# Kernel tuning notes

Hardware: AMD Instinct MI355X
Metric: run time of the kernel (lower is better)

## Reference

```python
import jax, jax.numpy as jnp
import numpy as np

N_NODES = 100000
N_EDGES = 1000000
D_IN = 64
D_OUT = 64


def setup_inputs() -> dict:
    key = jax.random.key(0)
    k_feat, k_ei, k_ew, k_w, k_b = jax.random.split(key, 5)
    features = jax.random.normal(k_feat, (N_NODES, D_IN), dtype=jnp.float32)
    edge_index = jax.random.randint(k_ei, (2, N_EDGES), 0, N_NODES, dtype=jnp.int64)
    edge_weight = jax.random.uniform(k_ew, (N_EDGES,), dtype=jnp.float32)
    # nn.Linear(input_dim, output_dim): weight [out, in], bias [out]
    lim = 1.0 / np.sqrt(D_IN)
    W = jax.random.uniform(k_w, (D_OUT, D_IN), minval=-lim, maxval=lim, dtype=jnp.float32)
    b = jax.random.uniform(k_b, (D_OUT,), minval=-lim, maxval=lim, dtype=jnp.float32)
    return {"features": features, "edge_index": edge_index,
            "edge_weight": edge_weight, "W": W, "b": b}


def reference(features, edge_index, edge_weight, W, b):
    # gather source-node features and scale by edge weight: [E, F]
    messages = features[edge_index[0]] * edge_weight[:, None]
    # scatter-add into destination nodes (vectorized form of the per-column
    # scatter_add_ loop in the original): [N, F]
    aggregated = jax.ops.segment_sum(messages, edge_index[1],
                                     num_segments=features.shape[0])
    # residual + linear; dropout is identity in eval mode
    return (aggregated + features) @ W.T + b
```

## Files before the change

### kernel.cpp

```cpp
#include <hip/hip_runtime.h>

constexpr int N_NODES = 100000;
constexpr int N_EDGES = 1000000;
constexpr int D = 64;
constexpr int NTILES = (N_NODES + 1023) / 1024;
constexpr int CAP = 32;
constexpr int OVF_CAP = 65536;


__global__ __launch_bounds__(256) void build_k(
    const int*   __restrict__ ei,
    const float* __restrict__ ew,
    int*         __restrict__ cnt,
    unsigned*    __restrict__ buckets,
    int*         __restrict__ ovfCount,
    int4*        __restrict__ ovf)
{
    int e = blockIdx.x * 256 + threadIdx.x;
    if (e >= N_EDGES) return;
    int   src = ei[e];
    int   dst = ei[N_EDGES + e];
    float w   = ew[e];
    int pos = atomicAdd(&cnt[dst], 1);
    if (pos < CAP) {
        unsigned q = (unsigned)(w * 32767.0f + 0.5f);
        buckets[(size_t)dst * CAP + pos] = ((unsigned)src << 15) | q;
    } else {
        int oi = atomicAdd(ovfCount, 1);
        if (oi < OVF_CAP) ovf[oi] = make_int4(dst, src, __float_as_int(w), 0);
    }
}

__global__ __launch_bounds__(256) void agg_gemm_bucket_k(
    const float*    __restrict__ feat,
    const unsigned* __restrict__ buckets,
    const int*      __restrict__ cnt,
    const int*      __restrict__ ovfCount,
    const int4*     __restrict__ ovf,
    const float*    __restrict__ W,
    const float*    __restrict__ bias,
    float*          __restrict__ out)
{
    constexpr int PITCH = 68;
    constexpr int NPB = 16;
    __shared__ float Wl[D * PITCH];
    __shared__ float xs[NPB][D];

    int tid = threadIdx.x;
    for (int i = tid; i < D * D; i += 256)
        Wl[(i >> 6) * PITCH + (i & 63)] = W[i];

    int lane = tid & 63;
    int wv   = tid >> 6;
    int g    = lane >> 4;
    int sub  = lane & 15;

    int slot = wv * 4 + g;
    int n    = blockIdx.x * NPB + slot;

    float4 acc = *reinterpret_cast<const float4*>(feat + (size_t)n * D + sub * 4);

    int degRaw = cnt[n];
    int deg = degRaw > CAP ? CAP : degRaw;
    const unsigned* ep = buckets + (size_t)n * CAP;
#pragma unroll 2
    for (int j = 0; j < deg; ++j) {
        unsigned r = ep[j];
        float w  = (float)(r & 0x7FFFu) * (1.0f / 32767.0f);
        int   s  = (int)(r >> 15);
        float4 f = *reinterpret_cast<const float4*>(
            feat + (size_t)s * D + sub * 4);
        acc.x = fmaf(f.x, w, acc.x);
        acc.y = fmaf(f.y, w, acc.y);
        acc.z = fmaf(f.z, w, acc.z);
        acc.w = fmaf(f.w, w, acc.w);
    }
    if (degRaw > CAP) {
        int m = *ovfCount;
        if (m > OVF_CAP) m = OVF_CAP;
        for (int i = 0; i < m; ++i) {
            int4 r = ovf[i];
            if (r.x == n) {
                float w  = __int_as_float(r.z);
                float4 f = *reinterpret_cast<const float4*>(
                    feat + (size_t)r.y * D + sub * 4);
                acc.x = fmaf(f.x, w, acc.x);
                acc.y = fmaf(f.y, w, acc.y);
                acc.z = fmaf(f.z, w, acc.z);
                acc.w = fmaf(f.w, w, acc.w);
            }
        }
    }
    *reinterpret_cast<float4*>(&xs[slot][sub * 4]) = acc;
    __syncthreads();

    const float4* w4 = reinterpret_cast<const float4*>(&Wl[lane * PITCH]);
    const float4* x0 = reinterpret_cast<const float4*>(&xs[wv * 4 + 0][0]);
    const float4* x1 = reinterpret_cast<const float4*>(&xs[wv * 4 + 1][0]);
    const float4* x2 = reinterpret_cast<const float4*>(&xs[wv * 4 + 2][0]);
    const float4* x3 = reinterpret_cast<const float4*>(&xs[wv * 4 + 3][0]);
    float b = bias[lane];
    float a0 = b, a1 = b, a2 = b, a3 = b;
#pragma unroll
    for (int i = 0; i < 16; ++i) {
        float4 wq = w4[i];
        float4 v0 = x0[i];
        float4 v1 = x1[i];
        float4 v2 = x2[i];
        float4 v3 = x3[i];
        a0 += v0.x * wq.x + v0.y * wq.y + v0.z * wq.z + v0.w * wq.w;
        a1 += v1.x * wq.x + v1.y * wq.y + v1.z * wq.z + v1.w * wq.w;
        a2 += v2.x * wq.x + v2.y * wq.y + v2.z * wq.z + v2.w * wq.w;
        a3 += v3.x * wq.x + v3.y * wq.y + v3.z * wq.z + v3.w * wq.w;
    }
    int nb = blockIdx.x * NPB + wv * 4;
    out[(size_t)(nb + 0) * D + lane] = a0;
    out[(size_t)(nb + 1) * D + lane] = a1;
    out[(size_t)(nb + 2) * D + lane] = a2;
    out[(size_t)(nb + 3) * D + lane] = a3;
}


__global__ __launch_bounds__(256) void rank_k(
    const int* __restrict__ ei, int* __restrict__ cnt, int* __restrict__ rank)
{
    int e = blockIdx.x * 256 + threadIdx.x;
    if (e >= N_EDGES) return;
    rank[e] = atomicAdd(&cnt[ei[N_EDGES + e]], 1);
}

__global__ __launch_bounds__(256) void tile_sum_k(
    const int* __restrict__ counts, int* __restrict__ tileSums)
{
    __shared__ int red[256];
    int t = threadIdx.x;
    int base = blockIdx.x * 1024 + t * 4;
    int4 c = make_int4(0, 0, 0, 0);
    if (base + 3 < N_NODES) {
        c = *reinterpret_cast<const int4*>(counts + base);
    } else {
        if (base + 0 < N_NODES) c.x = counts[base + 0];
        if (base + 1 < N_NODES) c.y = counts[base + 1];
        if (base + 2 < N_NODES) c.z = counts[base + 2];
        if (base + 3 < N_NODES) c.w = counts[base + 3];
    }
    red[t] = c.x + c.y + c.z + c.w;
    __syncthreads();
    for (int d = 128; d > 0; d >>= 1) {
        if (t < d) red[t] += red[t + d];
        __syncthreads();
    }
    if (t == 0) tileSums[blockIdx.x] = red[0];
}

__global__ __launch_bounds__(128) void tile_scan_k(
    const int* __restrict__ tileSums, int* __restrict__ tileBase)
{
    __shared__ int s[128];
    int t = threadIdx.x;
    s[t] = (t < NTILES) ? tileSums[t] : 0;
    __syncthreads();
    for (int d = 1; d < 128; d <<= 1) {
        int v = (t >= d) ? s[t - d] : 0;
        __syncthreads();
        s[t] += v;
        __syncthreads();
    }
    if (t < NTILES) tileBase[t] = t ? s[t - 1] : 0;
}

__global__ __launch_bounds__(256) void scan_apply_k(
    int* __restrict__ counts, const int* __restrict__ tileBase,
    int* __restrict__ offsets)
{
    __shared__ int tsum[256];
    int t = threadIdx.x;
    int base = blockIdx.x * 1024 + t * 4;
    int4 c = make_int4(0, 0, 0, 0);
    bool full = (base + 3 < N_NODES);
    if (full) {
        c = *reinterpret_cast<const int4*>(counts + base);
    } else {
        if (base + 0 < N_NODES) c.x = counts[base + 0];
        if (base + 1 < N_NODES) c.y = counts[base + 1];
        if (base + 2 < N_NODES) c.z = counts[base + 2];
        if (base + 3 < N_NODES) c.w = counts[base + 3];
    }
    tsum[t] = c.x + c.y + c.z + c.w;
    __syncthreads();
    for (int d = 1; d < 256; d <<= 1) {
        int v = (t >= d) ? tsum[t - d] : 0;
        __syncthreads();
        tsum[t] += v;
        __syncthreads();
    }
    int run = tileBase[blockIdx.x] + (t ? tsum[t - 1] : 0);
    int4 o = make_int4(run, run + c.x, run + c.x + c.y, run + c.x + c.y + c.z);
    if (full) {
        *reinterpret_cast<int4*>(offsets + base) = o;
        *reinterpret_cast<int4*>(counts  + base) = o;
    } else {
        if (base + 0 < N_NODES) { offsets[base + 0] = o.x; counts[base + 0] = o.x; }
        if (base + 1 < N_NODES) { offsets[base + 1] = o.y; counts[base + 1] = o.y; }
        if (base + 2 < N_NODES) { offsets[base + 2] = o.z; counts[base + 2] = o.z; }
        if (base + 3 < N_NODES) { offsets[base + 3] = o.w; counts[base + 3] = o.w; }
    }
    if (blockIdx.x == 0 && t == 0) offsets[N_NODES] = N_EDGES;
}

__global__ __launch_bounds__(256) void place_k(
    const int*   __restrict__ ei,
    const float* __restrict__ ew,
    const int*   __restrict__ rank,
    const int*   __restrict__ offsets,
    int2*        __restrict__ sorted_e)
{
    int e = blockIdx.x * 256 + threadIdx.x;
    if (e >= N_EDGES) return;
    int dst = ei[N_EDGES + e];
    int pos = offsets[dst] + rank[e];
    sorted_e[pos] = make_int2(ei[e], __float_as_int(ew[e]));
}

__global__ __launch_bounds__(256) void agg_gemm_k(
    const float* __restrict__ feat,
    const int2*  __restrict__ sorted_e,
    const int*   __restrict__ offsets,
    const float* __restrict__ W,
    const float* __restrict__ bias,
    float*       __restrict__ out)
{
    constexpr int PITCH = 68;
    constexpr int NPB = 16;
    __shared__ float Wl[D * PITCH];
    __shared__ float xs[NPB][D];

    int tid = threadIdx.x;
    for (int i = tid; i < D * D; i += 256)
        Wl[(i >> 6) * PITCH + (i & 63)] = W[i];

    int lane = tid & 63;
    int wv   = tid >> 6;
    int g    = lane >> 4;
    int sub  = lane & 15;

    int slot = wv * 4 + g;
    int n    = blockIdx.x * NPB + slot;
    int lo = offsets[n], hi = offsets[n + 1];
    int deg = hi - lo;

    float4 acc = *reinterpret_cast<const float4*>(feat + (size_t)n * D + sub * 4);

    const int2* ep = sorted_e + lo;
#pragma unroll 2
    for (int j = 0; j < deg; ++j) {
        int2  er = ep[j];
        float w  = __int_as_float(er.y);
        float4 f = *reinterpret_cast<const float4*>(
            feat + (size_t)er.x * D + sub * 4);
        acc.x = fmaf(f.x, w, acc.x);
        acc.y = fmaf(f.y, w, acc.y);
        acc.z = fmaf(f.z, w, acc.z);
        acc.w = fmaf(f.w, w, acc.w);
    }
    *reinterpret_cast<float4*>(&xs[slot][sub * 4]) = acc;
    __syncthreads();

    const float4* w4 = reinterpret_cast<const float4*>(&Wl[lane * PITCH]);
    const float4* x0 = reinterpret_cast<const float4*>(&xs[wv * 4 + 0][0]);
    const float4* x1 = reinterpret_cast<const float4*>(&xs[wv * 4 + 1][0]);
    const float4* x2 = reinterpret_cast<const float4*>(&xs[wv * 4 + 2][0]);
    const float4* x3 = reinterpret_cast<const float4*>(&xs[wv * 4 + 3][0]);
    float b = bias[lane];
    float a0 = b, a1 = b, a2 = b, a3 = b;
#pragma unroll
    for (int i = 0; i < 16; ++i) {
        float4 wq = w4[i];
        float4 v0 = x0[i];
        float4 v1 = x1[i];
        float4 v2 = x2[i];
        float4 v3 = x3[i];
        a0 += v0.x * wq.x + v0.y * wq.y + v0.z * wq.z + v0.w * wq.w;
        a1 += v1.x * wq.x + v1.y * wq.y + v1.z * wq.z + v1.w * wq.w;
        a2 += v2.x * wq.x + v2.y * wq.y + v2.z * wq.z + v2.w * wq.w;
        a3 += v3.x * wq.x + v3.y * wq.y + v3.z * wq.z + v3.w * wq.w;
    }
    int nb = blockIdx.x * NPB + wv * 4;
    out[(size_t)(nb + 0) * D + lane] = a0;
    out[(size_t)(nb + 1) * D + lane] = a1;
    out[(size_t)(nb + 2) * D + lane] = a2;
    out[(size_t)(nb + 3) * D + lane] = a3;
}


__global__ __launch_bounds__(256) void scatter_k(
    const float* __restrict__ feat,
    const int*   __restrict__ ei,
    const float* __restrict__ ew,
    float*       __restrict__ agg)
{
    int gid = blockIdx.x * 256 + threadIdx.x;
    int e = gid >> 4;
    if (e >= N_EDGES) return;
    int c = (gid & 15) * 4;
    int   src = ei[e];
    int   dst = ei[N_EDGES + e];
    float w   = ew[e];
    float4 f = *reinterpret_cast<const float4*>(feat + (size_t)src * D + c);
    float* a = agg + (size_t)dst * D + c;
    atomicAdd(a + 0, f.x * w);
    atomicAdd(a + 1, f.y * w);
    atomicAdd(a + 2, f.z * w);
    atomicAdd(a + 3, f.w * w);
}

__global__ __launch_bounds__(256) void gemm_k(
    const float* __restrict__ agg,
    const float* __restrict__ feat,
    const float* __restrict__ W,
    const float* __restrict__ bias,
    float*       __restrict__ out)
{
    constexpr int PITCH = 68;
    __shared__ float Wl[D * PITCH];
    __shared__ float xs[4][D];
    int tid = threadIdx.x;
    for (int i = tid; i < D * D; i += 256)
        Wl[(i >> 6) * PITCH + (i & 63)] = W[i];
    int o  = tid & 63;
    int wv = tid >> 6;
    int n  = blockIdx.x * 4 + wv;
    float b = bias[o];
    if (n < N_NODES)
        xs[wv][o] = agg[(size_t)n * D + o] + feat[(size_t)n * D + o];
    __syncthreads();
    if (n >= N_NODES) return;
    const float4* x4 = reinterpret_cast<const float4*>(&xs[wv][0]);
    const float4* w4 = reinterpret_cast<const float4*>(&Wl[o * PITCH]);
    float acc = b;
#pragma unroll
    for (int i = 0; i < 16; ++i) {
        float4 xv = x4[i];
        float4 wq = w4[i];
        acc += xv.x * wq.x + xv.y * wq.y + xv.z * wq.z + xv.w * wq.w;
    }
    out[(size_t)n * D + o] = acc;
}


extern "C" void kernel_launch(void* const* d_in, const int* in_sizes, int n_in,
                              void* d_out, int out_size, void* d_ws, size_t ws_size,
                              hipStream_t stream) {
    const float* feat = (const float*)d_in[0];
    const int*   ei   = (const int*)d_in[1];
    const float* ew   = (const float*)d_in[2];
    const float* W    = (const float*)d_in[3];
    const float* b    = (const float*)d_in[4];
    float*       out  = (float*)d_out;

    constexpr size_t NPAD = 100352;

    constexpr size_t CNT_OFF    = 0;
    constexpr size_t BUCKET_OFF = NPAD * sizeof(int);
    constexpr size_t OVF_OFF    = BUCKET_OFF + (size_t)N_NODES * CAP * sizeof(unsigned);
    constexpr size_t WS_BUCKET  = OVF_OFF + (size_t)OVF_CAP * sizeof(int4);

    constexpr size_t OFFSET_OFF = NPAD * sizeof(int);
    constexpr size_t RANK_OFF   = 2 * NPAD * sizeof(int);
    constexpr size_t SORT_OFF   = RANK_OFF + (size_t)N_EDGES * sizeof(int);
    constexpr size_t WS_SORT    = SORT_OFF + (size_t)N_EDGES * sizeof(int2);

    if (ws_size >= WS_BUCKET) {
        int*      cnt      = (int*)((char*)d_ws + CNT_OFF);
        int*      ovfCount = cnt + 100104;
        unsigned* buckets  = (unsigned*)((char*)d_ws + BUCKET_OFF);
        int4*     ovf      = (int4*)((char*)d_ws + OVF_OFF);

        hipMemsetAsync(cnt, 0, (100104 + 1) * sizeof(int), stream);
        build_k<<<(N_EDGES + 255) / 256, 256, 0, stream>>>(
            ei, ew, cnt, buckets, ovfCount, ovf);
        agg_gemm_bucket_k<<<N_NODES / 16, 256, 0, stream>>>(
            feat, buckets, cnt, ovfCount, ovf, W, b, out);
    } else if (ws_size >= WS_SORT) {
        int*  cnt      = (int*)((char*)d_ws + CNT_OFF);
        int*  offsets  = (int*)((char*)d_ws + OFFSET_OFF);
        int*  rank     = (int*)((char*)d_ws + RANK_OFF);
        int2* sorted_e = (int2*)((char*)d_ws + SORT_OFF);
        int*  tileSums = cnt + 100096;
        int*  tileBase = cnt + 100224;

        hipMemsetAsync(cnt, 0, N_NODES * sizeof(int), stream);
        rank_k     <<<(N_EDGES + 255) / 256, 256, 0, stream>>>(ei, cnt, rank);
        tile_sum_k <<<NTILES, 256, 0, stream>>>(cnt, tileSums);
        tile_scan_k<<<1, 128, 0, stream>>>(tileSums, tileBase);
        scan_apply_k<<<NTILES, 256, 0, stream>>>(cnt, tileBase, offsets);
        place_k    <<<(N_EDGES + 255) / 256, 256, 0, stream>>>(ei, ew, rank, offsets, sorted_e);
        agg_gemm_k <<<N_NODES / 16, 256, 0, stream>>>(feat, sorted_e, offsets, W, b, out);
    } else {
        const size_t agg_bytes = (size_t)N_NODES * D * sizeof(float);
        float* agg = (ws_size >= agg_bytes) ? (float*)d_ws : out;
        hipMemsetAsync(agg, 0, agg_bytes, stream);
        scatter_k<<<(N_EDGES * 16) / 256, 256, 0, stream>>>(feat, ei, ew, agg);
        gemm_k<<<(N_NODES + 3) / 4, 256, 0, stream>>>(agg, feat, W, b, out);
    }
}
```

Measured before the change: 210.0 us.

## Partition bucket build by destination range per XCD and split buckets into two halves

The build kernel becomes a grid-stride loop of 512 blocks. Each group of blocks (blockIdx mod 8) handles only edges whose destination falls in its 12500-node range. The intent is to keep the count atomics and bucket writes for a node range within one XCD's L2, reducing cross-die atomic and coherence traffic. The 32-slot per-node bucket is also split into a primary 16-slot array and a secondary 16-slot array, so the common low-degree case touches a denser 64-byte bucket. In exchange, every group reads the full destination index array (8x reads of that array), and the scheme relies on round-robin block-to-XCD dispatch.

```diff
diff --git a/kernel.cpp b/kernel.cpp
--- a/kernel.cpp
+++ b/kernel.cpp
@@ -4,36 +4,50 @@
 constexpr int N_EDGES = 1000000;
 constexpr int D = 64;
 constexpr int NTILES = (N_NODES + 1023) / 1024;
-constexpr int CAP = 32;
+constexpr int CAP1 = 16;
+constexpr int CAP2 = 16;
 constexpr int OVF_CAP = 65536;
+constexpr int NXCD = 8;
+constexpr int NODES_PER_GRP = 12500;
 
 
 __global__ __launch_bounds__(256) void build_k(
     const int*   __restrict__ ei,
     const float* __restrict__ ew,
     int*         __restrict__ cnt,
-    unsigned*    __restrict__ buckets,
+    unsigned*    __restrict__ b16,
+    unsigned*    __restrict__ b32,
     int*         __restrict__ ovfCount,
     int4*        __restrict__ ovf)
 {
-    int e = blockIdx.x * 256 + threadIdx.x;
-    if (e >= N_EDGES) return;
-    int   src = ei[e];
-    int   dst = ei[N_EDGES + e];
-    float w   = ew[e];
-    int pos = atomicAdd(&cnt[dst], 1);
-    if (pos < CAP) {
-        unsigned q = (unsigned)(w * 32767.0f + 0.5f);
-        buckets[(size_t)dst * CAP + pos] = ((unsigned)src << 15) | q;
-    } else {
-        int oi = atomicAdd(ovfCount, 1);
-        if (oi < OVF_CAP) ovf[oi] = make_int4(dst, src, __float_as_int(w), 0);
+    int grp  = blockIdx.x & 7;
+    int gidx = blockIdx.x >> 3;
+    int lo   = grp * NODES_PER_GRP;
+    int hi   = lo + NODES_PER_GRP;
+    int stride = (gridDim.x >> 3) * 256;
+
+    for (int e = gidx * 256 + threadIdx.x; e < N_EDGES; e += stride) {
+        int dst = ei[N_EDGES + e];
+        if (dst < lo || dst >= hi) continue;
+        int   src = ei[e];
+        float w   = ew[e];
+        unsigned rec = ((unsigned)src << 15) | (unsigned)(w * 32767.0f + 0.5f);
+        int pos = atomicAdd(&cnt[dst], 1);
+        if (pos < CAP1) {
+            b16[dst * 16 + pos] = rec;
+        } else if (pos < CAP1 + CAP2) {
+            b32[dst * 16 + (pos - CAP1)] = rec;
+        } else {
+            int oi = atomicAdd(ovfCount, 1);
+            if (oi < OVF_CAP) ovf[oi] = make_int4(dst, src, __float_as_int(w), 0);
+        }
     }
 }
 
 __global__ __launch_bounds__(256) void agg_gemm_bucket_k(
     const float*    __restrict__ feat,
-    const unsigned* __restrict__ buckets,
+    const unsigned* __restrict__ b16,
+    const unsigned* __restrict__ b32,
     const int*      __restrict__ cnt,
     const int*      __restrict__ ovfCount,
     const int4*     __restrict__ ovf,
@@ -61,8 +75,8 @@
     float4 acc = *reinterpret_cast<const float4*>(feat + (size_t)n * D + sub * 4);
 
     int degRaw = cnt[n];
-    int deg = degRaw > CAP ? CAP : degRaw;
-    const unsigned* ep = buckets + (size_t)n * CAP;
+    int deg = degRaw > CAP1 ? CAP1 : degRaw;
+    const unsigned* ep = b16 + (size_t)n * 16;
 #pragma unroll 2
     for (int j = 0; j < deg; ++j) {
         unsigned r = ep[j];
@@ -75,19 +89,34 @@
         acc.z = fmaf(f.z, w, acc.z);
         acc.w = fmaf(f.w, w, acc.w);
     }
-    if (degRaw > CAP) {
-        int m = *ovfCount;
-        if (m > OVF_CAP) m = OVF_CAP;
-        for (int i = 0; i < m; ++i) {
-            int4 r = ovf[i];
-            if (r.x == n) {
-                float w  = __int_as_float(r.z);
-                float4 f = *reinterpret_cast<const float4*>(
-                    feat + (size_t)r.y * D + sub * 4);
-                acc.x = fmaf(f.x, w, acc.x);
-                acc.y = fmaf(f.y, w, acc.y);
-                acc.z = fmaf(f.z, w, acc.z);
-                acc.w = fmaf(f.w, w, acc.w);
+    if (degRaw > CAP1) {
+        int d2 = (degRaw > CAP1 + CAP2 ? CAP1 + CAP2 : degRaw) - CAP1;
+        const unsigned* ep2 = b32 + (size_t)n * 16;
+        for (int j = 0; j < d2; ++j) {
+            unsigned r = ep2[j];
+            float w  = (float)(r & 0x7FFFu) * (1.0f / 32767.0f);
+            int   s  = (int)(r >> 15);
+            float4 f = *reinterpret_cast<const float4*>(
+                feat + (size_t)s * D + sub * 4);
+            acc.x = fmaf(f.x, w, acc.x);
+            acc.y = fmaf(f.y, w, acc.y);
+            acc.z = fmaf(f.z, w, acc.z);
+            acc.w = fmaf(f.w, w, acc.w);
+        }
+        if (degRaw > CAP1 + CAP2) {
+            int m = *ovfCount;
+            if (m > OVF_CAP) m = OVF_CAP;
+            for (int i = 0; i < m; ++i) {
+                int4 r = ovf[i];
+                if (r.x == n) {
+                    float w  = __int_as_float(r.z);
+                    float4 f = *reinterpret_cast<const float4*>(
+                        feat + (size_t)r.y * D + sub * 4);
+                    acc.x = fmaf(f.x, w, acc.x);
+                    acc.y = fmaf(f.y, w, acc.y);
+                    acc.z = fmaf(f.z, w, acc.z);
+                    acc.w = fmaf(f.w, w, acc.w);
+                }
             }
         }
     }
@@ -360,10 +389,11 @@
 
     constexpr size_t NPAD = 100352;
 
-    constexpr size_t CNT_OFF    = 0;
-    constexpr size_t BUCKET_OFF = NPAD * sizeof(int);
-    constexpr size_t OVF_OFF    = BUCKET_OFF + (size_t)N_NODES * CAP * sizeof(unsigned);
-    constexpr size_t WS_BUCKET  = OVF_OFF + (size_t)OVF_CAP * sizeof(int4);
+    constexpr size_t CNT_OFF   = 0;
+    constexpr size_t B16_OFF   = NPAD * sizeof(int);
+    constexpr size_t B32_OFF   = B16_OFF + (size_t)N_NODES * 16 * sizeof(unsigned);
+    constexpr size_t OVF_OFF   = B32_OFF + (size_t)N_NODES * 16 * sizeof(unsigned);
+    constexpr size_t WS_BUCKET = OVF_OFF + (size_t)OVF_CAP * sizeof(int4);
 
     constexpr size_t OFFSET_OFF = NPAD * sizeof(int);
     constexpr size_t RANK_OFF   = 2 * NPAD * sizeof(int);
@@ -373,14 +403,14 @@
     if (ws_size >= WS_BUCKET) {
         int*      cnt      = (int*)((char*)d_ws + CNT_OFF);
         int*      ovfCount = cnt + 100104;
-        unsigned* buckets  = (unsigned*)((char*)d_ws + BUCKET_OFF);
+        unsigned* b16      = (unsigned*)((char*)d_ws + B16_OFF);
+        unsigned* b32      = (unsigned*)((char*)d_ws + B32_OFF);
         int4*     ovf      = (int4*)((char*)d_ws + OVF_OFF);
 
         hipMemsetAsync(cnt, 0, (100104 + 1) * sizeof(int), stream);
-        build_k<<<(N_EDGES + 255) / 256, 256, 0, stream>>>(
-            ei, ew, cnt, buckets, ovfCount, ovf);
+        build_k<<<512, 256, 0, stream>>>(ei, ew, cnt, b16, b32, ovfCount, ovf);
         agg_gemm_bucket_k<<<N_NODES / 16, 256, 0, stream>>>(
-            feat, buckets, cnt, ovfCount, ovf, W, b, out);
+            feat, b16, b32, cnt, ovfCount, ovf, W, b, out);
     } else if (ws_size >= WS_SORT) {
         int*  cnt      = (int*)((char*)d_ws + CNT_OFF);
         int*  offsets  = (int*)((char*)d_ws + OFFSET_OFF);
```

Result: faster. 197.3 us (-6.0%).
